# Performance work log

Measured on AMD Instinct MI355X. Metric: run time of the kernel, lower is better.

Reference implementation:

```python
import jax, jax.numpy as jnp
import numpy as np

B, S, D = 1, 2048, 4096
H, HKV, HD = 64, 4, 64
REP = H // HKV
EPS = 1e-5
ROPE_BASE = 10000.0


def setup_inputs() -> dict:
    key = jax.random.key(0)
    ks = jax.random.split(key, 6)
    x = jax.random.normal(ks[0], (B, S, D), dtype=jnp.float32)
    wq = jax.random.normal(ks[1], (D, H * HD), dtype=jnp.float32) * 0.02
    wk = jax.random.normal(ks[2], (D, HKV * HD), dtype=jnp.float32) * 0.02
    wv = jax.random.normal(ks[3], (D, HKV * HD), dtype=jnp.float32) * 0.02
    wo = jax.random.normal(ks[4], (H * HD, D), dtype=jnp.float32) * 0.02
    q_norm_w = jnp.ones((HD,), dtype=jnp.float32)
    k_norm_w = jnp.ones((HD,), dtype=jnp.float32)
    # rotary tables: freqs_cis[t, j] = exp(i * t / base^(2j/head_dim))
    inv_freq = 1.0 / (ROPE_BASE ** (np.arange(0, HD, 2, dtype=np.float32) / HD))
    angles = np.arange(S, dtype=np.float32)[:, None] * inv_freq[None, :]  # [S, HD//2]
    freqs_cos = jnp.asarray(np.cos(angles), dtype=jnp.float32)
    freqs_sin = jnp.asarray(np.sin(angles), dtype=jnp.float32)
    return {"x": x, "wq": wq, "wk": wk, "wv": wv, "wo": wo,
            "q_norm_w": q_norm_w, "k_norm_w": k_norm_w,
            "freqs_cos": freqs_cos, "freqs_sin": freqs_sin}


def _rms_norm(x, w):
    # mean-of-squares over last dim (head_dim)
    ms = jnp.mean(jnp.square(x), axis=-1, keepdims=True)
    return w * (x * jax.lax.rsqrt(ms + EPS))


def _rope(x, cos, sin):
    # x: [B, S, nH, HD]; pairs of consecutive channels form complex numbers
    xr = x.reshape(*x.shape[:-1], HD // 2, 2)
    re, im = xr[..., 0], xr[..., 1]
    c = cos[None, :, None, :]  # [1, S, 1, HD//2]
    s = sin[None, :, None, :]
    out = jnp.stack([re * c - im * s, re * s + im * c], axis=-1)
    return out.reshape(x.shape)


def reference(x, wq, wk, wv, wo, q_norm_w, k_norm_w, freqs_cos, freqs_sin):
    bsz, seqlen, _ = x.shape
    xq = (x @ wq).reshape(bsz, seqlen, H, HD)
    xk = (x @ wk).reshape(bsz, seqlen, HKV, HD)
    xv = (x @ wv).reshape(bsz, seqlen, HKV, HD)
    xq = _rms_norm(xq, q_norm_w)
    xk = _rms_norm(xk, k_norm_w)
    xq = _rope(xq, freqs_cos, freqs_sin)
    xk = _rope(xk, freqs_cos, freqs_sin)
    # GQA: q head h maps to kv head h // REP (repeat_interleave semantics)
    q = xq.reshape(bsz, seqlen, HKV, REP, HD)  # [B, Sq, G, R, d]
    scale = 1.0 / jnp.sqrt(jnp.float32(HD))
    scores = jnp.einsum('bqgrd,bkgd->bgrqk', q, xk) * scale  # [B, G, R, Sq, Sk]
    causal = jnp.tril(jnp.ones((seqlen, seqlen), dtype=bool))
    scores = jnp.where(causal[None, None, None], scores, jnp.float32(-jnp.inf))
    probs = jax.nn.softmax(scores, axis=-1)
    out = jnp.einsum('bgrqk,bkgd->bqgrd', probs, xv)  # [B, Sq, G, R, d]
    out = out.reshape(bsz, seqlen, H * HD)
    return out @ wo
```

## Files before the change

kernel.cpp:

```cpp
#include <hip/hip_runtime.h>
#include <hip/hip_bf16.h>

typedef unsigned short u16;
typedef unsigned int   u32;
typedef __attribute__((ext_vector_type(8))) __bf16 bf16x8;
typedef __attribute__((ext_vector_type(4))) float  f32x4;
typedef __attribute__((ext_vector_type(8))) u16    u16x8;
typedef __attribute__((ext_vector_type(4))) u16    u16x4;
typedef __attribute__((ext_vector_type(2))) u32    u32x2;
typedef __attribute__((ext_vector_type(4))) u32    u32x4;

#define S_LEN 2048
#define DMODEL 4096
#define NH 64
#define NKV 4
#define HD 64

__device__ __forceinline__ u16 f2bf(float f) {
  u32 u = __builtin_bit_cast(u32, f);
  u32 r = (u + 0x7FFFu + ((u >> 16) & 1u)) >> 16;
  return (u16)r;
}
__device__ __forceinline__ u16 bfc(float f) {
  return __builtin_bit_cast(u16, (__bf16)f);
}
__device__ __forceinline__ u32 pk2(float lo, float hi) {
  return (u32)bfc(lo) | ((u32)bfc(hi) << 16);
}
__device__ __forceinline__ float bf2f(u16 u) {
  return __builtin_bit_cast(float, (u32)u << 16);
}
__device__ __forceinline__ float ex2(float x) { return __builtin_amdgcn_exp2f(x); }

__device__ __forceinline__ void gll16(const void* g, void* l) {
  __builtin_amdgcn_global_load_lds(
      (__attribute__((address_space(1))) void*)g,
      (__attribute__((address_space(3))) void*)l, 16, 0, 0);
}

__global__ __launch_bounds__(256) void cvt_f32_bf16_v4(const float* __restrict__ in,
                                                       u16* __restrict__ out) {
  const int i = blockIdx.x * 256 + threadIdx.x;
  float4 f = ((const float4*)in)[i];
  u16x4 u = { f2bf(f.x), f2bf(f.y), f2bf(f.z), f2bf(f.w) };
  *(u16x4*)&out[(size_t)i * 4] = u;
}

__global__ __launch_bounds__(256) void tconvs(const float* __restrict__ in,
                                              const float* __restrict__ in2, int istride,
                                              u16* __restrict__ out, int R, int C) {
  __shared__ __align__(16) float tile[32][36];
  const int nc = C >> 5;
  const int cb = blockIdx.x % nc, rb = blockIdx.x / nc;
  const int r = threadIdx.x >> 3, c4 = (threadIdx.x & 7) << 2;
  const size_t idx = (size_t)(rb * 32 + r) * istride + cb * 32 + c4;
  float4 v = *(const float4*)&in[idx];
  if (in2) {
    float4 u = *(const float4*)&in2[idx];
    v.x += u.x; v.y += u.y; v.z += u.z; v.w += u.w;
  }
  *(float4*)&tile[r][c4] = v;
  __syncthreads();
  const int orow = r, oc4 = c4;
  u32x2 pr;
  pr[0] = pk2(tile[oc4 + 0][orow], tile[oc4 + 1][orow]);
  pr[1] = pk2(tile[oc4 + 2][orow], tile[oc4 + 3][orow]);
  *(u32x2*)&out[(size_t)(cb * 32 + orow) * R + rb * 32 + oc4] = pr;
}

__global__ __launch_bounds__(256) void norm_rope(const float* __restrict__ in,
                                                 const float* __restrict__ in2,
                                                 int in_stride, int nheads,
                                                 const float* __restrict__ nw,
                                                 const float* __restrict__ cosT,
                                                 const float* __restrict__ sinT,
                                                 u16* __restrict__ outp, int out_stride,
                                                 float oscale) {
  const int wid = blockIdx.x * 4 + (threadIdx.x >> 6);
  const int l = threadIdx.x & 63;
  const int s = wid / nheads, h = wid - s * nheads;
  const size_t idx = (size_t)s * in_stride + h * 64 + l;
  const float v = in[idx] + in2[idx];
  float sq = v * v;
#pragma unroll
  for (int off = 32; off; off >>= 1) sq += __shfl_xor(sq, off, 64);
  const float rr = rsqrtf(sq * (1.f / 64.f) + 1e-5f);
  const float vn = v * rr * nw[l];
  const float p = __shfl_xor(vn, 1, 64);
  const int i2 = l >> 1;
  const float c = cosT[(size_t)s * 32 + i2];
  const float sn = sinT[(size_t)s * 32 + i2];
  const float o = ((l & 1) ? fmaf(p, sn, vn * c) : fmaf(-p, sn, vn * c)) * oscale;
  outp[(size_t)s * out_stride + h * 64 + l] = f2bf(o);
}

__global__ __launch_bounds__(256) void norm_rope_q(const u16* __restrict__ in,
                                                   int in_stride, int nheads,
                                                   const float* __restrict__ nw,
                                                   const float* __restrict__ cosT,
                                                   const float* __restrict__ sinT,
                                                   u16* __restrict__ outp, int out_stride,
                                                   float oscale) {
  const int wid = blockIdx.x * 4 + (threadIdx.x >> 6);
  const int l = threadIdx.x & 63;
  const int s = wid / nheads, h = wid - s * nheads;
  const size_t idx = (size_t)s * in_stride + h * 64 + l;
  const float v = bf2f(in[idx]);
  float sq = v * v;
#pragma unroll
  for (int off = 32; off; off >>= 1) sq += __shfl_xor(sq, off, 64);
  const float rr = rsqrtf(sq * (1.f / 64.f) + 1e-5f);
  const float vn = v * rr * nw[l];
  const float p = __shfl_xor(vn, 1, 64);
  const int i2 = l >> 1;
  const float c = cosT[(size_t)s * 32 + i2];
  const float sn = sinT[(size_t)s * 32 + i2];
  const float o = ((l & 1) ? fmaf(p, sn, vn * c) : fmaf(-p, sn, vn * c)) * oscale;
  outp[(size_t)s * out_stride + h * 64 + l] = f2bf(o);
}

__global__ __launch_bounds__(256) void gemm_kv(const u16* __restrict__ A,
                                               const u16* __restrict__ Bt,
                                               float* __restrict__ C0,
                                               float* __restrict__ C1,
                                               int M, int N, int K) {
  __shared__ __align__(16) u16 As[128 * 32];
  __shared__ __align__(16) u16 Bs[128 * 32];
  int bid = blockIdx.x;
  const int cpx = gridDim.x >> 3;
  bid = (bid & 7) * cpx + (bid >> 3);
  const int nbn = N >> 7;
  const int pertile = (M >> 7) * nbn;
  const int sl = bid / pertile;
  const int rem = bid - sl * pertile;
  const int bm = rem / nbn, bn = rem % nbn;
  const int m0 = bm << 7, n0 = bn << 7;
  const int tid = threadIdx.x;
  const int w = tid >> 6, l = tid & 63;
  const int wr = w >> 1, wc = w & 1;
  f32x4 acc[4][4] = {};

  const int Khalf = K >> 1;
  const int kbase = sl * Khalf;

  const char* Ag = (const char*)A +
      ((size_t)(m0 + w * 32 + (l >> 2)) * K + kbase + (l & 3) * 8) * 2;
  const char* Bg = (const char*)Bt +
      ((size_t)(n0 + w * 32 + (l >> 2)) * K + kbase + (l & 3) * 8) * 2;
  char* Al = (char*)As + (w * 32) * 64;
  char* Bl = (char*)Bs + (w * 32) * 64;
  const size_t rowadv = (size_t)16 * K * 2;

  for (int k0 = 0; k0 < Khalf; k0 += 32) {
    gll16(Ag, Al);
    gll16(Ag + rowadv, Al + 1024);
    gll16(Bg, Bl);
    gll16(Bg + rowadv, Bl + 1024);
    Ag += 64; Bg += 64;
    __syncthreads();
    bf16x8 af[4], bq[4];
#pragma unroll
    for (int i = 0; i < 4; ++i) {
      af[i] = *(const bf16x8*)&As[(wr * 64 + i * 16 + (l & 15)) * 32 + (l >> 4) * 8];
      bq[i] = *(const bf16x8*)&Bs[(wc * 64 + i * 16 + (l & 15)) * 32 + (l >> 4) * 8];
    }
#pragma unroll
    for (int mi = 0; mi < 4; ++mi)
#pragma unroll
      for (int ni = 0; ni < 4; ++ni)
        acc[mi][ni] = __builtin_amdgcn_mfma_f32_16x16x32_bf16(af[mi], bq[ni], acc[mi][ni], 0, 0, 0);
    __syncthreads();
  }
  float* Cs = sl ? C1 : C0;
  const int r0 = (l >> 4) * 4, c0 = l & 15;
#pragma unroll
  for (int mi = 0; mi < 4; ++mi)
#pragma unroll
    for (int ni = 0; ni < 4; ++ni)
#pragma unroll
      for (int r = 0; r < 4; ++r)
        Cs[(size_t)(m0 + wr * 64 + mi * 16 + r0 + r) * N + (n0 + wc * 64 + ni * 16 + c0)] =
            acc[mi][ni][r];
}

template <int BF16OUT>
__global__ __launch_bounds__(512, 2) void gemm_mn(const u16* __restrict__ A,
                                                  const u16* __restrict__ Bt,
                                                  void* __restrict__ Cout,
                                                  int M, int N, int K) {
  extern __shared__ __align__(16) char lds[];
  int bid = blockIdx.x;
  const int cpx = gridDim.x >> 3;
  bid = (bid & 7) * cpx + (bid >> 3);
  const int nbn = N >> 7;
  const int bm = bid / nbn, bn = bid % nbn;
  const int m0 = bm << 8, n0 = bn << 7;
  const int t = threadIdx.x, w = t >> 6, l = t & 63;
  const int wr = w >> 1, wc = w & 1;
  const int lr = l & 15, lg = l >> 4;

  const int sR = t >> 3, slot = t & 7;
  const int su = slot ^ (sR & 7);
  const int d1 = sR * 128 + slot * 16;
  const u16* Ag = A + (size_t)(m0 + 2 * sR + (su >> 2)) * K + (su & 3) * 8;
  const u16* Bg = Bt + (size_t)(n0 + 2 * sR + (su >> 2)) * K + (su & 3) * 8;
  const size_t r128 = (size_t)128 * K;

  f32x4 acc[4][4] = {};
  const int NPH = K >> 5;

  auto stage = [&](int ph) {
    const int kofs = ph * 32;
    char* pb = lds + (ph & 3) * 24576;
    gll16(Ag + kofs, pb + d1);
    gll16(Ag + r128 + kofs, pb + 8192 + d1);
    gll16(Bg + kofs, pb + 16384 + d1);
  };
  stage(0);
  stage(1);
  stage(2);

  const int sfrag = ((lr & 1) << 2) | lg;
  const int swz = (sfrag ^ ((lr >> 1) & 7)) << 4;
  const int aoff = (wr * 32 + (lr >> 1)) * 128 + swz;
  const int boff = 16384 + (wc * 32 + (lr >> 1)) * 128 + swz;

  auto compute = [&](int ph) {
    const char* base = lds + (ph & 3) * 24576;
    bf16x8 a[4], b[4];
#pragma unroll
    for (int mf = 0; mf < 4; ++mf) a[mf] = *(const bf16x8*)(base + aoff + mf * 1024);
#pragma unroll
    for (int nf = 0; nf < 4; ++nf) b[nf] = *(const bf16x8*)(base + boff + nf * 1024);
    __builtin_amdgcn_s_setprio(1);
#pragma unroll
    for (int mf = 0; mf < 4; ++mf)
#pragma unroll
      for (int nf = 0; nf < 4; ++nf)
        acc[mf][nf] = __builtin_amdgcn_mfma_f32_16x16x32_bf16(a[mf], b[nf], acc[mf][nf], 0, 0, 0);
    __builtin_amdgcn_s_setprio(0);
    asm volatile("" ::: "memory");
  };

#pragma unroll 4
  for (int ph = 0; ph < NPH - 3; ++ph) {
    __builtin_amdgcn_sched_barrier(0);
    asm volatile("s_waitcnt vmcnt(6)" ::: "memory");
    __builtin_amdgcn_s_barrier();
    stage(ph + 3);
    compute(ph);
  }
  __builtin_amdgcn_sched_barrier(0);
  asm volatile("s_waitcnt vmcnt(6)" ::: "memory");
  __builtin_amdgcn_s_barrier();
  compute(NPH - 3);
  __builtin_amdgcn_sched_barrier(0);
  asm volatile("s_waitcnt vmcnt(3)" ::: "memory");
  __builtin_amdgcn_s_barrier();
  compute(NPH - 2);
  __builtin_amdgcn_sched_barrier(0);
  asm volatile("s_waitcnt vmcnt(0)" ::: "memory");
  __builtin_amdgcn_s_barrier();
  compute(NPH - 1);

#pragma unroll
  for (int mf = 0; mf < 4; ++mf)
#pragma unroll
    for (int nf = 0; nf < 4; ++nf)
#pragma unroll
      for (int rr = 0; rr < 4; ++rr) {
        const size_t cidx = (size_t)(m0 + wr * 64 + mf * 16 + lg * 4 + rr) * N +
                            (n0 + wc * 64 + nf * 16 + lr);
        if (BF16OUT)
          ((u16*)Cout)[cidx] = bfc(acc[mf][nf][rr]);
        else
          ((float*)Cout)[cidx] = acc[mf][nf][rr];
      }
}

__global__ __launch_bounds__(256) void attn_fwd(const u16* __restrict__ Q,
                                                const u16* __restrict__ Kb,
                                                const u16* __restrict__ VT,
                                                u16* __restrict__ O) {
  const int h = blockIdx.x & 63;
  const int qb = (S_LEN / 64 - 1) - (blockIdx.x >> 6);
  const int kvh = h >> 4;
  __shared__ __align__(16) char KV[2 * 16384];
  const int tid = threadIdx.x;
  const int w = tid >> 6, l = tid & 63;
  const int lr = l & 15, lg = l >> 4;

  const int srow = w * 16 + (l >> 3);
  const int s0 = (l & 7) ^ (srow & 7);
  const int sv = (s0 & 4) | ((s0 & 1) << 1) | ((s0 & 2) >> 1);
  const char* Kg = (const char*)Kb + kvh * 128 + (size_t)srow * 512 + s0 * 16;
  const char* Vg = (const char*)VT + (size_t)(kvh * 64 + srow) * (S_LEN * 2) + sv * 16;
  const int wofs = w * 2048;

  auto stage = [&](int page) {
    char* pb = KV + page * 16384 + wofs;
    gll16(Kg, pb);
    gll16(Kg + 8 * 512, pb + 1024);
    gll16(Vg, pb + 8192);
    gll16(Vg + 8 * (S_LEN * 2), pb + 8192 + 1024);
    Kg += 64 * 512;
    Vg += 128;
  };

  bf16x8 qf[2];
  {
    const size_t qoff = (size_t)(qb * 64 + w * 16 + lr) * DMODEL + h * HD + lg * 8;
    qf[0] = *(const bf16x8*)&Q[qoff];
    qf[1] = *(const bf16x8*)&Q[qoff + 32];
  }
  f32x4 o[4] = {};
  float lrow = 0.f;
  const int qlane = qb * 64 + w * 16 + lr;
  const int abase = (l & 48) | ((l >> 2) & 12);

  const int xr = lr & 7;
  const int kb0 = lr * 128 + ((lg ^ xr) << 4);
  const int kb1 = lr * 128 + (((4 + lg) ^ xr) << 4);
  const int vb0 = 8192 + kb0;
  const int vb1 = 8192 + kb1;

  stage(0);

  for (int t = 0; t <= qb; ++t) {
    __builtin_amdgcn_sched_barrier(0);
    asm volatile("s_waitcnt vmcnt(0)" ::: "memory");
    __builtin_amdgcn_s_barrier();
    __builtin_amdgcn_sched_barrier(0);
    if (t < qb) stage((t + 1) & 1);
    const char* page = KV + (t & 1) * 16384;

    f32x4 sf[4] = {};
#pragma unroll
    for (int ni = 0; ni < 4; ++ni) {
      bf16x8 kf0 = *(const bf16x8*)(page + kb0 + ni * 2048);
      bf16x8 kf1 = *(const bf16x8*)(page + kb1 + ni * 2048);
      sf[ni] = __builtin_amdgcn_mfma_f32_16x16x32_bf16(kf0, qf[0], sf[ni], 0, 0, 0);
      sf[ni] = __builtin_amdgcn_mfma_f32_16x16x32_bf16(kf1, qf[1], sf[ni], 0, 0, 0);
    }
    if (t == qb) {
      const int kvb = t * 64 + lg * 4;
#pragma unroll
      for (int ni = 0; ni < 4; ++ni)
#pragma unroll
        for (int r = 0; r < 4; ++r)
          if (kvb + ni * 16 + r > qlane) sf[ni][r] = -1e30f;
    }
    float p[4][4];
    float r4[4];
#pragma unroll
    for (int ni = 0; ni < 4; ++ni) {
#pragma unroll
      for (int r = 0; r < 4; ++r) p[ni][r] = ex2(sf[ni][r]);
      r4[ni] = (p[ni][0] + p[ni][1]) + (p[ni][2] + p[ni][3]);
    }
    float rs = (r4[0] + r4[1]) + (r4[2] + r4[3]);
    rs += __shfl_xor(rs, 16, 64);
    rs += __shfl_xor(rs, 32, 64);
    lrow += rs;

    const bool odd = (lg & 1);
#pragma unroll
    for (int kk = 0; kk < 2; ++kk) {
      const int nA = 2 * kk, nB = 2 * kk + 1;
      const u32 cA0 = pk2(p[nA][0], p[nA][1]), cA1 = pk2(p[nA][2], p[nA][3]);
      const u32 cB0 = pk2(p[nB][0], p[nB][1]), cB1 = pk2(p[nB][2], p[nB][3]);
      const u32 cS0 = odd ? cB0 : cA0, cS1 = odd ? cB1 : cA1;
      const u32 cP0 = odd ? cA0 : cB0, cP1 = odd ? cA1 : cB1;
      const u32 rP0 = (u32)__shfl_xor((int)cP0, 16, 64);
      const u32 rP1 = (u32)__shfl_xor((int)cP1, 16, 64);
      u32x4 wv;
      wv[0] = odd ? rP0 : cS0;
      wv[1] = odd ? rP1 : cS1;
      wv[2] = odd ? cS0 : rP0;
      wv[3] = odd ? cS1 : rP1;
      const bf16x8 pa = __builtin_bit_cast(bf16x8, wv);
      const int vb = kk ? vb1 : vb0;
#pragma unroll
      for (int ni = 0; ni < 4; ++ni) {
        bf16x8 vf = *(const bf16x8*)(page + vb + ni * 2048);
        o[ni] = __builtin_amdgcn_mfma_f32_16x16x32_bf16(pa, vf, o[ni], 0, 0, 0);
      }
    }
  }
  const float lv0 = __shfl(lrow, abase + 0, 64);
  const float lv1 = __shfl(lrow, abase + 1, 64);
  const float lv2 = __shfl(lrow, abase + 2, 64);
  const float lv3 = __shfl(lrow, abase + 3, 64);
  const f32x4 lv = {lv0, lv1, lv2, lv3};
#pragma unroll
  for (int ni = 0; ni < 4; ++ni)
#pragma unroll
    for (int r = 0; r < 4; ++r) {
      const size_t orow = (size_t)(qb * 64 + w * 16 + lg * 4 + r);
      O[orow * DMODEL + h * HD + ni * 16 + lr] = f2bf(o[ni][r] / lv[r]);
    }
}

extern "C" void kernel_launch(void* const* d_in, const int* in_sizes, int n_in,
                              void* d_out, int out_size, void* d_ws, size_t ws_size,
                              hipStream_t stream) {
  const float* x   = (const float*)d_in[0];
  const float* wq  = (const float*)d_in[1];
  const float* wk  = (const float*)d_in[2];
  const float* wv  = (const float*)d_in[3];
  const float* wo  = (const float*)d_in[4];
  const float* qnw = (const float*)d_in[5];
  const float* knw = (const float*)d_in[6];
  const float* fc  = (const float*)d_in[7];
  const float* fs  = (const float*)d_in[8];
  float* out = (float*)d_out;

  char* ws = (char*)d_ws;
  size_t off = 0;
  auto alloc = [&](size_t bytes) {
    char* p = ws + off;
    off += (bytes + 255) & ~(size_t)255;
    return p;
  };
  u16*   xb    = (u16*)alloc((size_t)S_LEN * DMODEL * 2);
  u16*   wqT   = (u16*)alloc((size_t)DMODEL * DMODEL * 2);
  u16*   wkvT  = (u16*)alloc((size_t)512 * DMODEL * 2);
  u16*   woT   = (u16*)alloc((size_t)DMODEL * DMODEL * 2);
  u16*   Pq    = (u16*)alloc((size_t)S_LEN * DMODEL * 2);
  float* KV0   = (float*)alloc((size_t)S_LEN * 512 * 4);
  float* KV1   = (float*)alloc((size_t)S_LEN * 512 * 4);
  u16*   Qn    = (u16*)alloc((size_t)S_LEN * DMODEL * 2);
  u16*   Kn    = (u16*)alloc((size_t)S_LEN * 256 * 2);
  u16*   VTb   = (u16*)alloc((size_t)256 * S_LEN * 2);
  u16*   Ob    = (u16*)alloc((size_t)S_LEN * DMODEL * 2);

  hipFuncSetAttribute((const void*)gemm_mn<1>, hipFuncAttributeMaxDynamicSharedMemorySize, 98304);
  hipFuncSetAttribute((const void*)gemm_mn<0>, hipFuncAttributeMaxDynamicSharedMemorySize, 98304);

  cvt_f32_bf16_v4<<<(S_LEN * DMODEL / 4) / 256, 256, 0, stream>>>(x, xb);
  tconvs<<<(4096 / 32) * (4096 / 32), 256, 0, stream>>>(wq, nullptr, 4096, wqT, 4096, 4096);
  tconvs<<<(4096 / 32) * (256 / 32), 256, 0, stream>>>(wk, nullptr, 256, wkvT, 4096, 256);
  tconvs<<<(4096 / 32) * (256 / 32), 256, 0, stream>>>(wv, nullptr, 256,
      wkvT + (size_t)256 * 4096, 4096, 256);
  tconvs<<<(4096 / 32) * (4096 / 32), 256, 0, stream>>>(wo, nullptr, 4096, woT, 4096, 4096);

  gemm_mn<1><<<(2048 / 256) * (4096 / 128), 512, 98304, stream>>>(
      xb, wqT, Pq, 2048, 4096, 4096);
  gemm_kv<<<2 * (2048 / 128) * (512 / 128), 256, 0, stream>>>(
      xb, wkvT, KV0, KV1, 2048, 512, 4096);

  const float QSCALE = 0.125f * 1.44269504088896340736f;
  norm_rope_q<<<(S_LEN * NH) / 4, 256, 0, stream>>>(Pq, DMODEL, NH, qnw, fc, fs,
                                                    Qn, DMODEL, QSCALE);
  norm_rope<<<(S_LEN * NKV) / 4, 256, 0, stream>>>(KV0, KV1, 512, NKV,
                                                   knw, fc, fs, Kn, 256, 1.0f);
  tconvs<<<(2048 / 32) * (256 / 32), 256, 0, stream>>>(KV0 + 256, KV1 + 256, 512,
                                                       VTb, 2048, 256);

  attn_fwd<<<(S_LEN / 64) * NH, 256, 0, stream>>>(Qn, Kn, VTb, Ob);

  gemm_mn<0><<<(2048 / 256) * (4096 / 128), 512, 98304, stream>>>(
      Ob, woT, out, 2048, 4096, 4096);
}
```

Baseline: 332.7 us.

## Fuse Q/K/V projections into one GEMM and shrink GEMM tile to 128x128

Concatenates the transposed wq, wk and wv into one weight matrix so a single gemm_mn launch produces Q, K and V in bf16, replacing the separate split-K fp32 gemm_kv and its two partial-sum buffers. K normalisation now reuses norm_rope_q, and V is transposed by a new bf16 tconvb kernel. The gemm_mn tile drops from 256x128 to 128x128 with smaller LDS stages, which gives more blocks for the larger N. The trade is that K/V are rounded to bf16 before norm and RoPE, and each block loads the B tile with less reuse.

```diff
diff --git a/kernel.cpp b/kernel.cpp
--- a/kernel.cpp
+++ b/kernel.cpp
@@ -46,52 +46,32 @@
   *(u16x4*)&out[(size_t)i * 4] = u;
 }
 
-__global__ __launch_bounds__(256) void tconvs(const float* __restrict__ in,
-                                              const float* __restrict__ in2, int istride,
+__global__ __launch_bounds__(256) void tconvs(const float* __restrict__ in, int istride,
                                               u16* __restrict__ out, int R, int C) {
   __shared__ __align__(16) float tile[32][36];
   const int nc = C >> 5;
   const int cb = blockIdx.x % nc, rb = blockIdx.x / nc;
   const int r = threadIdx.x >> 3, c4 = (threadIdx.x & 7) << 2;
-  const size_t idx = (size_t)(rb * 32 + r) * istride + cb * 32 + c4;
-  float4 v = *(const float4*)&in[idx];
-  if (in2) {
-    float4 u = *(const float4*)&in2[idx];
-    v.x += u.x; v.y += u.y; v.z += u.z; v.w += u.w;
-  }
+  float4 v = *(const float4*)&in[(size_t)(rb * 32 + r) * istride + cb * 32 + c4];
   *(float4*)&tile[r][c4] = v;
   __syncthreads();
-  const int orow = r, oc4 = c4;
   u32x2 pr;
-  pr[0] = pk2(tile[oc4 + 0][orow], tile[oc4 + 1][orow]);
-  pr[1] = pk2(tile[oc4 + 2][orow], tile[oc4 + 3][orow]);
-  *(u32x2*)&out[(size_t)(cb * 32 + orow) * R + rb * 32 + oc4] = pr;
-}
-
-__global__ __launch_bounds__(256) void norm_rope(const float* __restrict__ in,
-                                                 const float* __restrict__ in2,
-                                                 int in_stride, int nheads,
-                                                 const float* __restrict__ nw,
-                                                 const float* __restrict__ cosT,
-                                                 const float* __restrict__ sinT,
-                                                 u16* __restrict__ outp, int out_stride,
-                                                 float oscale) {
-  const int wid = blockIdx.x * 4 + (threadIdx.x >> 6);
-  const int l = threadIdx.x & 63;
-  const int s = wid / nheads, h = wid - s * nheads;
-  const size_t idx = (size_t)s * in_stride + h * 64 + l;
-  const float v = in[idx] + in2[idx];
-  float sq = v * v;
-#pragma unroll
-  for (int off = 32; off; off >>= 1) sq += __shfl_xor(sq, off, 64);
-  const float rr = rsqrtf(sq * (1.f / 64.f) + 1e-5f);
-  const float vn = v * rr * nw[l];
-  const float p = __shfl_xor(vn, 1, 64);
-  const int i2 = l >> 1;
-  const float c = cosT[(size_t)s * 32 + i2];
-  const float sn = sinT[(size_t)s * 32 + i2];
-  const float o = ((l & 1) ? fmaf(p, sn, vn * c) : fmaf(-p, sn, vn * c)) * oscale;
-  outp[(size_t)s * out_stride + h * 64 + l] = f2bf(o);
+  pr[0] = pk2(tile[c4 + 0][r], tile[c4 + 1][r]);
+  pr[1] = pk2(tile[c4 + 2][r], tile[c4 + 3][r]);
+  *(u32x2*)&out[(size_t)(cb * 32 + r) * R + rb * 32 + c4] = pr;
+}
+
+__global__ __launch_bounds__(256) void tconvb(const u16* __restrict__ in, int istride,
+                                              u16* __restrict__ out, int R, int C) {
+  __shared__ __align__(16) u16 tile[32][40];
+  const int nc = C >> 5;
+  const int cb = blockIdx.x % nc, rb = blockIdx.x / nc;
+  const int r = threadIdx.x >> 3, c4 = (threadIdx.x & 7) << 2;
+  u16x4 v = *(const u16x4*)&in[(size_t)(rb * 32 + r) * istride + cb * 32 + c4];
+  *(u16x4*)&tile[r][c4] = v;
+  __syncthreads();
+  u16x4 o = { tile[c4 + 0][r], tile[c4 + 1][r], tile[c4 + 2][r], tile[c4 + 3][r] };
+  *(u16x4*)&out[(size_t)(cb * 32 + r) * R + rb * 32 + c4] = o;
 }
 
 __global__ __launch_bounds__(256) void norm_rope_q(const u16* __restrict__ in,
@@ -119,70 +99,6 @@
   outp[(size_t)s * out_stride + h * 64 + l] = f2bf(o);
 }
 
-__global__ __launch_bounds__(256) void gemm_kv(const u16* __restrict__ A,
-                                               const u16* __restrict__ Bt,
-                                               float* __restrict__ C0,
-                                               float* __restrict__ C1,
-                                               int M, int N, int K) {
-  __shared__ __align__(16) u16 As[128 * 32];
-  __shared__ __align__(16) u16 Bs[128 * 32];
-  int bid = blockIdx.x;
-  const int cpx = gridDim.x >> 3;
-  bid = (bid & 7) * cpx + (bid >> 3);
-  const int nbn = N >> 7;
-  const int pertile = (M >> 7) * nbn;
-  const int sl = bid / pertile;
-  const int rem = bid - sl * pertile;
-  const int bm = rem / nbn, bn = rem % nbn;
-  const int m0 = bm << 7, n0 = bn << 7;
-  const int tid = threadIdx.x;
-  const int w = tid >> 6, l = tid & 63;
-  const int wr = w >> 1, wc = w & 1;
-  f32x4 acc[4][4] = {};
-
-  const int Khalf = K >> 1;
-  const int kbase = sl * Khalf;
-
-  const char* Ag = (const char*)A +
-      ((size_t)(m0 + w * 32 + (l >> 2)) * K + kbase + (l & 3) * 8) * 2;
-  const char* Bg = (const char*)Bt +
-      ((size_t)(n0 + w * 32 + (l >> 2)) * K + kbase + (l & 3) * 8) * 2;
-  char* Al = (char*)As + (w * 32) * 64;
-  char* Bl = (char*)Bs + (w * 32) * 64;
-  const size_t rowadv = (size_t)16 * K * 2;
-
-  for (int k0 = 0; k0 < Khalf; k0 += 32) {
-    gll16(Ag, Al);
-    gll16(Ag + rowadv, Al + 1024);
-    gll16(Bg, Bl);
-    gll16(Bg + rowadv, Bl + 1024);
-    Ag += 64; Bg += 64;
-    __syncthreads();
-    bf16x8 af[4], bq[4];
-#pragma unroll
-    for (int i = 0; i < 4; ++i) {
-      af[i] = *(const bf16x8*)&As[(wr * 64 + i * 16 + (l & 15)) * 32 + (l >> 4) * 8];
-      bq[i] = *(const bf16x8*)&Bs[(wc * 64 + i * 16 + (l & 15)) * 32 + (l >> 4) * 8];
-    }
-#pragma unroll
-    for (int mi = 0; mi < 4; ++mi)
-#pragma unroll
-      for (int ni = 0; ni < 4; ++ni)
-        acc[mi][ni] = __builtin_amdgcn_mfma_f32_16x16x32_bf16(af[mi], bq[ni], acc[mi][ni], 0, 0, 0);
-    __syncthreads();
-  }
-  float* Cs = sl ? C1 : C0;
-  const int r0 = (l >> 4) * 4, c0 = l & 15;
-#pragma unroll
-  for (int mi = 0; mi < 4; ++mi)
-#pragma unroll
-    for (int ni = 0; ni < 4; ++ni)
-#pragma unroll
-      for (int r = 0; r < 4; ++r)
-        Cs[(size_t)(m0 + wr * 64 + mi * 16 + r0 + r) * N + (n0 + wc * 64 + ni * 16 + c0)] =
-            acc[mi][ni][r];
-}
-
 template <int BF16OUT>
 __global__ __launch_bounds__(512, 2) void gemm_mn(const u16* __restrict__ A,
                                                   const u16* __restrict__ Bt,
@@ -194,7 +110,7 @@
   bid = (bid & 7) * cpx + (bid >> 3);
   const int nbn = N >> 7;
   const int bm = bid / nbn, bn = bid % nbn;
-  const int m0 = bm << 8, n0 = bn << 7;
+  const int m0 = bm << 7, n0 = bn << 7;
   const int t = threadIdx.x, w = t >> 6, l = t & 63;
   const int wr = w >> 1, wc = w & 1;
   const int lr = l & 15, lg = l >> 4;
@@ -204,17 +120,15 @@
   const int d1 = sR * 128 + slot * 16;
   const u16* Ag = A + (size_t)(m0 + 2 * sR + (su >> 2)) * K + (su & 3) * 8;
   const u16* Bg = Bt + (size_t)(n0 + 2 * sR + (su >> 2)) * K + (su & 3) * 8;
-  const size_t r128 = (size_t)128 * K;
-
-  f32x4 acc[4][4] = {};
+
+  f32x4 acc[2][4] = {};
   const int NPH = K >> 5;
 
   auto stage = [&](int ph) {
     const int kofs = ph * 32;
-    char* pb = lds + (ph & 3) * 24576;
+    char* pb = lds + (ph & 3) * 16384;
     gll16(Ag + kofs, pb + d1);
-    gll16(Ag + r128 + kofs, pb + 8192 + d1);
-    gll16(Bg + kofs, pb + 16384 + d1);
+    gll16(Bg + kofs, pb + 8192 + d1);
   };
   stage(0);
   stage(1);
@@ -222,19 +136,19 @@
 
   const int sfrag = ((lr & 1) << 2) | lg;
   const int swz = (sfrag ^ ((lr >> 1) & 7)) << 4;
-  const int aoff = (wr * 32 + (lr >> 1)) * 128 + swz;
-  const int boff = 16384 + (wc * 32 + (lr >> 1)) * 128 + swz;
+  const int aoff = (wr * 16 + (lr >> 1)) * 128 + swz;
+  const int boff = 8192 + (wc * 32 + (lr >> 1)) * 128 + swz;
 
   auto compute = [&](int ph) {
-    const char* base = lds + (ph & 3) * 24576;
-    bf16x8 a[4], b[4];
-#pragma unroll
-    for (int mf = 0; mf < 4; ++mf) a[mf] = *(const bf16x8*)(base + aoff + mf * 1024);
+    const char* base = lds + (ph & 3) * 16384;
+    bf16x8 a[2], b[4];
+#pragma unroll
+    for (int mf = 0; mf < 2; ++mf) a[mf] = *(const bf16x8*)(base + aoff + mf * 1024);
 #pragma unroll
     for (int nf = 0; nf < 4; ++nf) b[nf] = *(const bf16x8*)(base + boff + nf * 1024);
     __builtin_amdgcn_s_setprio(1);
 #pragma unroll
-    for (int mf = 0; mf < 4; ++mf)
+    for (int mf = 0; mf < 2; ++mf)
 #pragma unroll
       for (int nf = 0; nf < 4; ++nf)
         acc[mf][nf] = __builtin_amdgcn_mfma_f32_16x16x32_bf16(a[mf], b[nf], acc[mf][nf], 0, 0, 0);
@@ -245,17 +159,17 @@
 #pragma unroll 4
   for (int ph = 0; ph < NPH - 3; ++ph) {
     __builtin_amdgcn_sched_barrier(0);
-    asm volatile("s_waitcnt vmcnt(6)" ::: "memory");
+    asm volatile("s_waitcnt vmcnt(4)" ::: "memory");
     __builtin_amdgcn_s_barrier();
     stage(ph + 3);
     compute(ph);
   }
   __builtin_amdgcn_sched_barrier(0);
-  asm volatile("s_waitcnt vmcnt(6)" ::: "memory");
+  asm volatile("s_waitcnt vmcnt(4)" ::: "memory");
   __builtin_amdgcn_s_barrier();
   compute(NPH - 3);
   __builtin_amdgcn_sched_barrier(0);
-  asm volatile("s_waitcnt vmcnt(3)" ::: "memory");
+  asm volatile("s_waitcnt vmcnt(2)" ::: "memory");
   __builtin_amdgcn_s_barrier();
   compute(NPH - 2);
   __builtin_amdgcn_sched_barrier(0);
@@ -264,12 +178,12 @@
   compute(NPH - 1);
 
 #pragma unroll
-  for (int mf = 0; mf < 4; ++mf)
+  for (int mf = 0; mf < 2; ++mf)
 #pragma unroll
     for (int nf = 0; nf < 4; ++nf)
 #pragma unroll
       for (int rr = 0; rr < 4; ++rr) {
-        const size_t cidx = (size_t)(m0 + wr * 64 + mf * 16 + lg * 4 + rr) * N +
+        const size_t cidx = (size_t)(m0 + wr * 32 + mf * 16 + lg * 4 + rr) * N +
                             (n0 + wc * 64 + nf * 16 + lr);
         if (BF16OUT)
           ((u16*)Cout)[cidx] = bfc(acc[mf][nf][rr]);
@@ -422,43 +336,39 @@
     off += (bytes + 255) & ~(size_t)255;
     return p;
   };
+  const int NQKV = DMODEL + 512;
   u16*   xb    = (u16*)alloc((size_t)S_LEN * DMODEL * 2);
-  u16*   wqT   = (u16*)alloc((size_t)DMODEL * DMODEL * 2);
-  u16*   wkvT  = (u16*)alloc((size_t)512 * DMODEL * 2);
+  u16*   wqkvT = (u16*)alloc((size_t)NQKV * DMODEL * 2);
   u16*   woT   = (u16*)alloc((size_t)DMODEL * DMODEL * 2);
-  u16*   Pq    = (u16*)alloc((size_t)S_LEN * DMODEL * 2);
-  float* KV0   = (float*)alloc((size_t)S_LEN * 512 * 4);
-  float* KV1   = (float*)alloc((size_t)S_LEN * 512 * 4);
+  u16*   Pq    = (u16*)alloc((size_t)S_LEN * NQKV * 2);
   u16*   Qn    = (u16*)alloc((size_t)S_LEN * DMODEL * 2);
   u16*   Kn    = (u16*)alloc((size_t)S_LEN * 256 * 2);
   u16*   VTb   = (u16*)alloc((size_t)256 * S_LEN * 2);
   u16*   Ob    = (u16*)alloc((size_t)S_LEN * DMODEL * 2);
 
-  hipFuncSetAttribute((const void*)gemm_mn<1>, hipFuncAttributeMaxDynamicSharedMemorySize, 98304);
-  hipFuncSetAttribute((const void*)gemm_mn<0>, hipFuncAttributeMaxDynamicSharedMemorySize, 98304);
+  hipFuncSetAttribute((const void*)gemm_mn<1>, hipFuncAttributeMaxDynamicSharedMemorySize, 65536);
+  hipFuncSetAttribute((const void*)gemm_mn<0>, hipFuncAttributeMaxDynamicSharedMemorySize, 65536);
 
   cvt_f32_bf16_v4<<<(S_LEN * DMODEL / 4) / 256, 256, 0, stream>>>(x, xb);
-  tconvs<<<(4096 / 32) * (4096 / 32), 256, 0, stream>>>(wq, nullptr, 4096, wqT, 4096, 4096);
-  tconvs<<<(4096 / 32) * (256 / 32), 256, 0, stream>>>(wk, nullptr, 256, wkvT, 4096, 256);
-  tconvs<<<(4096 / 32) * (256 / 32), 256, 0, stream>>>(wv, nullptr, 256,
-      wkvT + (size_t)256 * 4096, 4096, 256);
-  tconvs<<<(4096 / 32) * (4096 / 32), 256, 0, stream>>>(wo, nullptr, 4096, woT, 4096, 4096);
-
-  gemm_mn<1><<<(2048 / 256) * (4096 / 128), 512, 98304, stream>>>(
-      xb, wqT, Pq, 2048, 4096, 4096);
-  gemm_kv<<<2 * (2048 / 128) * (512 / 128), 256, 0, stream>>>(
-      xb, wkvT, KV0, KV1, 2048, 512, 4096);
+  tconvs<<<(4096 / 32) * (4096 / 32), 256, 0, stream>>>(wq, 4096, wqkvT, 4096, 4096);
+  tconvs<<<(4096 / 32) * (256 / 32), 256, 0, stream>>>(wk, 256,
+      wqkvT + (size_t)4096 * 4096, 4096, 256);
+  tconvs<<<(4096 / 32) * (256 / 32), 256, 0, stream>>>(wv, 256,
+      wqkvT + (size_t)4352 * 4096, 4096, 256);
+  tconvs<<<(4096 / 32) * (4096 / 32), 256, 0, stream>>>(wo, 4096, woT, 4096, 4096);
+
+  gemm_mn<1><<<(2048 / 128) * (NQKV / 128), 512, 65536, stream>>>(
+      xb, wqkvT, Pq, 2048, NQKV, 4096);
 
   const float QSCALE = 0.125f * 1.44269504088896340736f;
-  norm_rope_q<<<(S_LEN * NH) / 4, 256, 0, stream>>>(Pq, DMODEL, NH, qnw, fc, fs,
+  norm_rope_q<<<(S_LEN * NH) / 4, 256, 0, stream>>>(Pq, NQKV, NH, qnw, fc, fs,
                                                     Qn, DMODEL, QSCALE);
-  norm_rope<<<(S_LEN * NKV) / 4, 256, 0, stream>>>(KV0, KV1, 512, NKV,
-                                                   knw, fc, fs, Kn, 256, 1.0f);
-  tconvs<<<(2048 / 32) * (256 / 32), 256, 0, stream>>>(KV0 + 256, KV1 + 256, 512,
-                                                       VTb, 2048, 256);
+  norm_rope_q<<<(S_LEN * NKV) / 4, 256, 0, stream>>>(Pq + 4096, NQKV, NKV,
+                                                     knw, fc, fs, Kn, 256, 1.0f);
+  tconvb<<<(2048 / 32) * (256 / 32), 256, 0, stream>>>(Pq + 4352, NQKV, VTb, 2048, 256);
 
   attn_fwd<<<(S_LEN / 64) * NH, 256, 0, stream>>>(Qn, Kn, VTb, Ob);
 
-  gemm_mn<0><<<(2048 / 256) * (4096 / 128), 512, 98304, stream>>>(
+  gemm_mn<0><<<(2048 / 128) * (4096 / 128), 512, 65536, stream>>>(
       Ob, woT, out, 2048, 4096, 4096);
 }
```

New measurement: 358.0 us. 1.08x slower.

## Double K-step per stage in GEMM pipeline with three 48KB LDS buffers

Applied to the files above, without the earlier changes.

Restructures the gemm_mn main loop so each pipeline stage loads and computes 64 K-elements (two 32-wide halves) instead of 32. It uses three LDS buffers of 48KB, raising dynamic shared memory to 144KB, with a fully unrolled, statically indexed buffer rotation that hardcodes K=4096. The aim is to halve the number of barriers and waitcnt syncs per K and to make each load batch larger. In exchange it uses more LDS and hardcodes the loop count, so it only works for K=4096. A small tconvs cleanup renames variables without changing behaviour.

```diff
diff --git a/kernel.cpp b/kernel.cpp
--- a/kernel.cpp
+++ b/kernel.cpp
@@ -61,11 +61,10 @@
   }
   *(float4*)&tile[r][c4] = v;
   __syncthreads();
-  const int orow = r, oc4 = c4;
   u32x2 pr;
-  pr[0] = pk2(tile[oc4 + 0][orow], tile[oc4 + 1][orow]);
-  pr[1] = pk2(tile[oc4 + 2][orow], tile[oc4 + 3][orow]);
-  *(u32x2*)&out[(size_t)(cb * 32 + orow) * R + rb * 32 + oc4] = pr;
+  pr[0] = pk2(tile[c4 + 0][r], tile[c4 + 1][r]);
+  pr[1] = pk2(tile[c4 + 2][r], tile[c4 + 3][r]);
+  *(u32x2*)&out[(size_t)(cb * 32 + r) * R + rb * 32 + c4] = pr;
 }
 
 __global__ __launch_bounds__(256) void norm_rope(const float* __restrict__ in,
@@ -207,26 +206,26 @@
   const size_t r128 = (size_t)128 * K;
 
   f32x4 acc[4][4] = {};
-  const int NPH = K >> 5;
-
-  auto stage = [&](int ph) {
-    const int kofs = ph * 32;
-    char* pb = lds + (ph & 3) * 24576;
-    gll16(Ag + kofs, pb + d1);
-    gll16(Ag + r128 + kofs, pb + 8192 + d1);
-    gll16(Bg + kofs, pb + 16384 + d1);
+
+  auto stage = [&](int ph, const int pg) {
+    const int k0 = ph * 64;
+    char* pb = lds + pg * 49152;
+    gll16(Ag + k0, pb + d1);
+    gll16(Ag + r128 + k0, pb + 8192 + d1);
+    gll16(Bg + k0, pb + 16384 + d1);
+    gll16(Ag + k0 + 32, pb + 24576 + d1);
+    gll16(Ag + r128 + k0 + 32, pb + 32768 + d1);
+    gll16(Bg + k0 + 32, pb + 40960 + d1);
   };
-  stage(0);
-  stage(1);
-  stage(2);
+  stage(0, 0);
+  stage(1, 1);
 
   const int sfrag = ((lr & 1) << 2) | lg;
   const int swz = (sfrag ^ ((lr >> 1) & 7)) << 4;
   const int aoff = (wr * 32 + (lr >> 1)) * 128 + swz;
   const int boff = 16384 + (wc * 32 + (lr >> 1)) * 128 + swz;
 
-  auto compute = [&](int ph) {
-    const char* base = lds + (ph & 3) * 24576;
+  auto half = [&](const char* base) {
     bf16x8 a[4], b[4];
 #pragma unroll
     for (int mf = 0; mf < 4; ++mf) a[mf] = *(const bf16x8*)(base + aoff + mf * 1024);
@@ -241,27 +240,30 @@
     __builtin_amdgcn_s_setprio(0);
     asm volatile("" ::: "memory");
   };
-
-#pragma unroll 4
-  for (int ph = 0; ph < NPH - 3; ++ph) {
-    __builtin_amdgcn_sched_barrier(0);
-    asm volatile("s_waitcnt vmcnt(6)" ::: "memory");
-    __builtin_amdgcn_s_barrier();
-    stage(ph + 3);
-    compute(ph);
+  auto compute = [&](const int pg) {
+    const char* base = lds + pg * 49152;
+    half(base);
+    half(base + 24576);
+  };
+
+#define SYNC6 __builtin_amdgcn_sched_barrier(0); \
+  asm volatile("s_waitcnt vmcnt(6)" ::: "memory"); \
+  __builtin_amdgcn_s_barrier();
+#define SYNC0 __builtin_amdgcn_sched_barrier(0); \
+  asm volatile("s_waitcnt vmcnt(0)" ::: "memory"); \
+  __builtin_amdgcn_s_barrier();
+
+  for (int b = 0; b < 60; b += 3) {
+    SYNC6; stage(b + 2, 2); compute(0);
+    SYNC6; stage(b + 3, 0); compute(1);
+    SYNC6; stage(b + 4, 1); compute(2);
   }
-  __builtin_amdgcn_sched_barrier(0);
-  asm volatile("s_waitcnt vmcnt(6)" ::: "memory");
-  __builtin_amdgcn_s_barrier();
-  compute(NPH - 3);
-  __builtin_amdgcn_sched_barrier(0);
-  asm volatile("s_waitcnt vmcnt(3)" ::: "memory");
-  __builtin_amdgcn_s_barrier();
-  compute(NPH - 2);
-  __builtin_amdgcn_sched_barrier(0);
-  asm volatile("s_waitcnt vmcnt(0)" ::: "memory");
-  __builtin_amdgcn_s_barrier();
-  compute(NPH - 1);
+  SYNC6; stage(62, 2); compute(0);
+  SYNC6; stage(63, 0); compute(1);
+  SYNC6; compute(2);
+  SYNC0; compute(0);
+#undef SYNC6
+#undef SYNC0
 
 #pragma unroll
   for (int mf = 0; mf < 4; ++mf)
@@ -434,8 +436,8 @@
   u16*   VTb   = (u16*)alloc((size_t)256 * S_LEN * 2);
   u16*   Ob    = (u16*)alloc((size_t)S_LEN * DMODEL * 2);
 
-  hipFuncSetAttribute((const void*)gemm_mn<1>, hipFuncAttributeMaxDynamicSharedMemorySize, 98304);
-  hipFuncSetAttribute((const void*)gemm_mn<0>, hipFuncAttributeMaxDynamicSharedMemorySize, 98304);
+  hipFuncSetAttribute((const void*)gemm_mn<1>, hipFuncAttributeMaxDynamicSharedMemorySize, 147456);
+  hipFuncSetAttribute((const void*)gemm_mn<0>, hipFuncAttributeMaxDynamicSharedMemorySize, 147456);
 
   cvt_f32_bf16_v4<<<(S_LEN * DMODEL / 4) / 256, 256, 0, stream>>>(x, xb);
   tconvs<<<(4096 / 32) * (4096 / 32), 256, 0, stream>>>(wq, nullptr, 4096, wqT, 4096, 4096);
@@ -444,7 +446,7 @@
       wkvT + (size_t)256 * 4096, 4096, 256);
   tconvs<<<(4096 / 32) * (4096 / 32), 256, 0, stream>>>(wo, nullptr, 4096, woT, 4096, 4096);
 
-  gemm_mn<1><<<(2048 / 256) * (4096 / 128), 512, 98304, stream>>>(
+  gemm_mn<1><<<(2048 / 256) * (4096 / 128), 512, 147456, stream>>>(
       xb, wqT, Pq, 2048, 4096, 4096);
   gemm_kv<<<2 * (2048 / 128) * (512 / 128), 256, 0, stream>>>(
       xb, wkvT, KV0, KV1, 2048, 512, 4096);
@@ -459,6 +461,6 @@
 
   attn_fwd<<<(S_LEN / 64) * NH, 256, 0, stream>>>(Qn, Kn, VTb, Ob);
 
-  gemm_mn<0><<<(2048 / 256) * (4096 / 128), 512, 98304, stream>>>(
+  gemm_mn<0><<<(2048 / 256) * (4096 / 128), 512, 147456, stream>>>(
       Ob, woT, out, 2048, 4096, 4096);
 }
```

Result: no change. 332.9 us (+0.1%).

## Use 256x256 split-K GEMM tiles with bf16 partials and priority hints in attention

Applied to the files above, without the earlier changes.

Replaces the 256x128 GEMM with a 256x256-tile kernel that splits K in two across blocks. Each half writes bf16 partial sums, so the grid stays at 256 blocks while per-block reuse goes up. Q-projection partials are summed inside the norm/rope kernel, and the output projection gets a new add kernel that combines its two bf16 partials into fp32. The attention MFMA sections also get s_setprio hints. The cost is extra partial-buffer traffic, an extra launch, and bf16 rounding of the partial sums before the final add, which lowers output precision.

```diff
diff --git a/kernel.cpp b/kernel.cpp
--- a/kernel.cpp
+++ b/kernel.cpp
@@ -44,6 +44,20 @@
   float4 f = ((const float4*)in)[i];
   u16x4 u = { f2bf(f.x), f2bf(f.y), f2bf(f.z), f2bf(f.w) };
   *(u16x4*)&out[(size_t)i * 4] = u;
+}
+
+__global__ __launch_bounds__(256) void addbf(float* __restrict__ out,
+                                             const u16* __restrict__ p0,
+                                             const u16* __restrict__ p1) {
+  const int i = blockIdx.x * 256 + threadIdx.x;
+  u16x4 a = *(const u16x4*)&p0[(size_t)i * 4];
+  u16x4 b = *(const u16x4*)&p1[(size_t)i * 4];
+  float4 o;
+  o.x = bf2f(a[0]) + bf2f(b[0]);
+  o.y = bf2f(a[1]) + bf2f(b[1]);
+  o.z = bf2f(a[2]) + bf2f(b[2]);
+  o.w = bf2f(a[3]) + bf2f(b[3]);
+  ((float4*)out)[i] = o;
 }
 
 __global__ __launch_bounds__(256) void tconvs(const float* __restrict__ in,
@@ -61,11 +75,10 @@
   }
   *(float4*)&tile[r][c4] = v;
   __syncthreads();
-  const int orow = r, oc4 = c4;
   u32x2 pr;
-  pr[0] = pk2(tile[oc4 + 0][orow], tile[oc4 + 1][orow]);
-  pr[1] = pk2(tile[oc4 + 2][orow], tile[oc4 + 3][orow]);
-  *(u32x2*)&out[(size_t)(cb * 32 + orow) * R + rb * 32 + oc4] = pr;
+  pr[0] = pk2(tile[c4 + 0][r], tile[c4 + 1][r]);
+  pr[1] = pk2(tile[c4 + 2][r], tile[c4 + 3][r]);
+  *(u32x2*)&out[(size_t)(cb * 32 + r) * R + rb * 32 + c4] = pr;
 }
 
 __global__ __launch_bounds__(256) void norm_rope(const float* __restrict__ in,
@@ -94,18 +107,19 @@
   outp[(size_t)s * out_stride + h * 64 + l] = f2bf(o);
 }
 
-__global__ __launch_bounds__(256) void norm_rope_q(const u16* __restrict__ in,
-                                                   int in_stride, int nheads,
-                                                   const float* __restrict__ nw,
-                                                   const float* __restrict__ cosT,
-                                                   const float* __restrict__ sinT,
-                                                   u16* __restrict__ outp, int out_stride,
-                                                   float oscale) {
+__global__ __launch_bounds__(256) void norm_rope_q2(const u16* __restrict__ in,
+                                                    const u16* __restrict__ in2,
+                                                    int in_stride, int nheads,
+                                                    const float* __restrict__ nw,
+                                                    const float* __restrict__ cosT,
+                                                    const float* __restrict__ sinT,
+                                                    u16* __restrict__ outp, int out_stride,
+                                                    float oscale) {
   const int wid = blockIdx.x * 4 + (threadIdx.x >> 6);
   const int l = threadIdx.x & 63;
   const int s = wid / nheads, h = wid - s * nheads;
   const size_t idx = (size_t)s * in_stride + h * 64 + l;
-  const float v = bf2f(in[idx]);
+  const float v = bf2f(in[idx]) + bf2f(in2[idx]);
   float sq = v * v;
 #pragma unroll
   for (int off = 32; off; off >>= 1) sq += __shfl_xor(sq, off, 64);
@@ -183,38 +197,45 @@
             acc[mi][ni][r];
 }
 
-template <int BF16OUT>
-__global__ __launch_bounds__(512, 2) void gemm_mn(const u16* __restrict__ A,
-                                                  const u16* __restrict__ Bt,
-                                                  void* __restrict__ Cout,
-                                                  int M, int N, int K) {
+__global__ __launch_bounds__(512, 2) void gemm8(const u16* __restrict__ A,
+                                                const u16* __restrict__ Bt,
+                                                u16* __restrict__ C0,
+                                                u16* __restrict__ C1,
+                                                int M, int N, int K) {
   extern __shared__ __align__(16) char lds[];
+  const int nbm = M >> 8, nbn = N >> 8;
   int bid = blockIdx.x;
   const int cpx = gridDim.x >> 3;
   bid = (bid & 7) * cpx + (bid >> 3);
-  const int nbn = N >> 7;
-  const int bm = bid / nbn, bn = bid % nbn;
-  const int m0 = bm << 8, n0 = bn << 7;
+  const int pertile = nbm * nbn;
+  const int sl = bid / pertile;
+  const int rem = bid - sl * pertile;
+  const int bm = rem / nbn, bn = rem % nbn;
+  const int m0 = bm << 8, n0 = bn << 8;
   const int t = threadIdx.x, w = t >> 6, l = t & 63;
-  const int wr = w >> 1, wc = w & 1;
+  const int wr = w >> 2, wc = w & 3;
   const int lr = l & 15, lg = l >> 4;
+
+  const int Khalf = K >> 1;
+  const int kbase = sl * Khalf;
 
   const int sR = t >> 3, slot = t & 7;
   const int su = slot ^ (sR & 7);
   const int d1 = sR * 128 + slot * 16;
-  const u16* Ag = A + (size_t)(m0 + 2 * sR + (su >> 2)) * K + (su & 3) * 8;
-  const u16* Bg = Bt + (size_t)(n0 + 2 * sR + (su >> 2)) * K + (su & 3) * 8;
+  const u16* Ag = A + (size_t)(m0 + 2 * sR + (su >> 2)) * K + kbase + (su & 3) * 8;
+  const u16* Bg = Bt + (size_t)(n0 + 2 * sR + (su >> 2)) * K + kbase + (su & 3) * 8;
   const size_t r128 = (size_t)128 * K;
 
-  f32x4 acc[4][4] = {};
-  const int NPH = K >> 5;
+  f32x4 acc[8][4] = {};
+  const int NPH = Khalf >> 5;
 
   auto stage = [&](int ph) {
     const int kofs = ph * 32;
-    char* pb = lds + (ph & 3) * 24576;
+    char* pb = lds + (ph & 3) * 32768;
     gll16(Ag + kofs, pb + d1);
     gll16(Ag + r128 + kofs, pb + 8192 + d1);
     gll16(Bg + kofs, pb + 16384 + d1);
+    gll16(Bg + r128 + kofs, pb + 24576 + d1);
   };
   stage(0);
   stage(1);
@@ -222,19 +243,19 @@
 
   const int sfrag = ((lr & 1) << 2) | lg;
   const int swz = (sfrag ^ ((lr >> 1) & 7)) << 4;
-  const int aoff = (wr * 32 + (lr >> 1)) * 128 + swz;
+  const int aoff = (wr * 64 + (lr >> 1)) * 128 + swz;
   const int boff = 16384 + (wc * 32 + (lr >> 1)) * 128 + swz;
 
   auto compute = [&](int ph) {
-    const char* base = lds + (ph & 3) * 24576;
-    bf16x8 a[4], b[4];
-#pragma unroll
-    for (int mf = 0; mf < 4; ++mf) a[mf] = *(const bf16x8*)(base + aoff + mf * 1024);
+    const char* base = lds + (ph & 3) * 32768;
+    bf16x8 a[8], b[4];
+#pragma unroll
+    for (int mf = 0; mf < 8; ++mf) a[mf] = *(const bf16x8*)(base + aoff + mf * 1024);
 #pragma unroll
     for (int nf = 0; nf < 4; ++nf) b[nf] = *(const bf16x8*)(base + boff + nf * 1024);
     __builtin_amdgcn_s_setprio(1);
 #pragma unroll
-    for (int mf = 0; mf < 4; ++mf)
+    for (int mf = 0; mf < 8; ++mf)
 #pragma unroll
       for (int nf = 0; nf < 4; ++nf)
         acc[mf][nf] = __builtin_amdgcn_mfma_f32_16x16x32_bf16(a[mf], b[nf], acc[mf][nf], 0, 0, 0);
@@ -245,17 +266,17 @@
 #pragma unroll 4
   for (int ph = 0; ph < NPH - 3; ++ph) {
     __builtin_amdgcn_sched_barrier(0);
-    asm volatile("s_waitcnt vmcnt(6)" ::: "memory");
+    asm volatile("s_waitcnt vmcnt(8)" ::: "memory");
     __builtin_amdgcn_s_barrier();
     stage(ph + 3);
     compute(ph);
   }
   __builtin_amdgcn_sched_barrier(0);
-  asm volatile("s_waitcnt vmcnt(6)" ::: "memory");
+  asm volatile("s_waitcnt vmcnt(8)" ::: "memory");
   __builtin_amdgcn_s_barrier();
   compute(NPH - 3);
   __builtin_amdgcn_sched_barrier(0);
-  asm volatile("s_waitcnt vmcnt(3)" ::: "memory");
+  asm volatile("s_waitcnt vmcnt(4)" ::: "memory");
   __builtin_amdgcn_s_barrier();
   compute(NPH - 2);
   __builtin_amdgcn_sched_barrier(0);
@@ -263,19 +284,15 @@
   __builtin_amdgcn_s_barrier();
   compute(NPH - 1);
 
-#pragma unroll
-  for (int mf = 0; mf < 4; ++mf)
+  u16* Cs = sl ? C1 : C0;
+#pragma unroll
+  for (int mf = 0; mf < 8; ++mf)
 #pragma unroll
     for (int nf = 0; nf < 4; ++nf)
 #pragma unroll
-      for (int rr = 0; rr < 4; ++rr) {
-        const size_t cidx = (size_t)(m0 + wr * 64 + mf * 16 + lg * 4 + rr) * N +
-                            (n0 + wc * 64 + nf * 16 + lr);
-        if (BF16OUT)
-          ((u16*)Cout)[cidx] = bfc(acc[mf][nf][rr]);
-        else
-          ((float*)Cout)[cidx] = acc[mf][nf][rr];
-      }
+      for (int rr = 0; rr < 4; ++rr)
+        Cs[(size_t)(m0 + wr * 128 + mf * 16 + lg * 4 + rr) * N +
+           (n0 + wc * 64 + nf * 16 + lr)] = bfc(acc[mf][nf][rr]);
 }
 
 __global__ __launch_bounds__(256) void attn_fwd(const u16* __restrict__ Q,
@@ -335,6 +352,7 @@
     const char* page = KV + (t & 1) * 16384;
 
     f32x4 sf[4] = {};
+    __builtin_amdgcn_s_setprio(1);
 #pragma unroll
     for (int ni = 0; ni < 4; ++ni) {
       bf16x8 kf0 = *(const bf16x8*)(page + kb0 + ni * 2048);
@@ -342,6 +360,7 @@
       sf[ni] = __builtin_amdgcn_mfma_f32_16x16x32_bf16(kf0, qf[0], sf[ni], 0, 0, 0);
       sf[ni] = __builtin_amdgcn_mfma_f32_16x16x32_bf16(kf1, qf[1], sf[ni], 0, 0, 0);
     }
+    __builtin_amdgcn_s_setprio(0);
     if (t == qb) {
       const int kvb = t * 64 + lg * 4;
 #pragma unroll
@@ -380,11 +399,13 @@
       wv[3] = odd ? cS1 : rP1;
       const bf16x8 pa = __builtin_bit_cast(bf16x8, wv);
       const int vb = kk ? vb1 : vb0;
+      __builtin_amdgcn_s_setprio(1);
 #pragma unroll
       for (int ni = 0; ni < 4; ++ni) {
         bf16x8 vf = *(const bf16x8*)(page + vb + ni * 2048);
         o[ni] = __builtin_amdgcn_mfma_f32_16x16x32_bf16(pa, vf, o[ni], 0, 0, 0);
       }
+      __builtin_amdgcn_s_setprio(0);
     }
   }
   const float lv0 = __shfl(lrow, abase + 0, 64);
@@ -426,16 +447,18 @@
   u16*   wqT   = (u16*)alloc((size_t)DMODEL * DMODEL * 2);
   u16*   wkvT  = (u16*)alloc((size_t)512 * DMODEL * 2);
   u16*   woT   = (u16*)alloc((size_t)DMODEL * DMODEL * 2);
-  u16*   Pq    = (u16*)alloc((size_t)S_LEN * DMODEL * 2);
+  u16*   Pq0   = (u16*)alloc((size_t)S_LEN * DMODEL * 2);
+  u16*   Pq1   = (u16*)alloc((size_t)S_LEN * DMODEL * 2);
   float* KV0   = (float*)alloc((size_t)S_LEN * 512 * 4);
   float* KV1   = (float*)alloc((size_t)S_LEN * 512 * 4);
   u16*   Qn    = (u16*)alloc((size_t)S_LEN * DMODEL * 2);
   u16*   Kn    = (u16*)alloc((size_t)S_LEN * 256 * 2);
   u16*   VTb   = (u16*)alloc((size_t)256 * S_LEN * 2);
   u16*   Ob    = (u16*)alloc((size_t)S_LEN * DMODEL * 2);
-
-  hipFuncSetAttribute((const void*)gemm_mn<1>, hipFuncAttributeMaxDynamicSharedMemorySize, 98304);
-  hipFuncSetAttribute((const void*)gemm_mn<0>, hipFuncAttributeMaxDynamicSharedMemorySize, 98304);
+  u16*   Op0   = Pq0;
+  u16*   Op1   = Pq1;
+
+  hipFuncSetAttribute((const void*)gemm8, hipFuncAttributeMaxDynamicSharedMemorySize, 131072);
 
   cvt_f32_bf16_v4<<<(S_LEN * DMODEL / 4) / 256, 256, 0, stream>>>(x, xb);
   tconvs<<<(4096 / 32) * (4096 / 32), 256, 0, stream>>>(wq, nullptr, 4096, wqT, 4096, 4096);
@@ -444,14 +467,14 @@
       wkvT + (size_t)256 * 4096, 4096, 256);
   tconvs<<<(4096 / 32) * (4096 / 32), 256, 0, stream>>>(wo, nullptr, 4096, woT, 4096, 4096);
 
-  gemm_mn<1><<<(2048 / 256) * (4096 / 128), 512, 98304, stream>>>(
-      xb, wqT, Pq, 2048, 4096, 4096);
+  gemm8<<<2 * (2048 / 256) * (4096 / 256), 512, 131072, stream>>>(
+      xb, wqT, Pq0, Pq1, 2048, 4096, 4096);
   gemm_kv<<<2 * (2048 / 128) * (512 / 128), 256, 0, stream>>>(
       xb, wkvT, KV0, KV1, 2048, 512, 4096);
 
   const float QSCALE = 0.125f * 1.44269504088896340736f;
-  norm_rope_q<<<(S_LEN * NH) / 4, 256, 0, stream>>>(Pq, DMODEL, NH, qnw, fc, fs,
-                                                    Qn, DMODEL, QSCALE);
+  norm_rope_q2<<<(S_LEN * NH) / 4, 256, 0, stream>>>(Pq0, Pq1, DMODEL, NH, qnw, fc, fs,
+                                                     Qn, DMODEL, QSCALE);
   norm_rope<<<(S_LEN * NKV) / 4, 256, 0, stream>>>(KV0, KV1, 512, NKV,
                                                    knw, fc, fs, Kn, 256, 1.0f);
   tconvs<<<(2048 / 32) * (256 / 32), 256, 0, stream>>>(KV0 + 256, KV1 + 256, 512,
@@ -459,6 +482,7 @@
 
   attn_fwd<<<(S_LEN / 64) * NH, 256, 0, stream>>>(Qn, Kn, VTb, Ob);
 
-  gemm_mn<0><<<(2048 / 256) * (4096 / 128), 512, 98304, stream>>>(
-      Ob, woT, out, 2048, 4096, 4096);
-}
+  gemm8<<<2 * (2048 / 256) * (4096 / 256), 512, 131072, stream>>>(
+      Ob, woT, Op0, Op1, 2048, 4096, 4096);
+  addbf<<<(S_LEN * DMODEL / 4) / 256, 256, 0, stream>>>(out, Op0, Op1);
+}
```

Result: no change. 337.7 us (+1.5%).
